# Optimization experiments

Measured on AMD Instinct MI355X. Metric: run time of the kernel, lower is better.

The kernel has to match this reference:

```python
import jax, jax.numpy as jnp
import numpy as np

GRAN = 4      # mask_spatial_granularity
STRIDE = 1    # dilate_stride
PAD = 1       # ExpandMask padding -> 3x3 all-ones dilation kernel


def setup_inputs() -> dict:
    key = jax.random.key(0)
    k1, k2, k3 = jax.random.split(key, 3)
    B, C, H, W = 32, 64, 112, 112
    G = 4
    mh, mw = H // STRIDE // GRAN, W // STRIDE // GRAN
    x = jax.random.normal(k1, (B, C, H, W), jnp.float32)
    weight = jax.random.normal(k2, (2 * G, C), jnp.float32) * 0.05  # 1x1 conv
    bias = jnp.zeros((2 * G,), jnp.float32).at[:G].set(5.0).at[G + 1:].set(1.0)
    # standard gumbel(0,1) noise for gumbel_softmax
    u = jax.random.uniform(k3, (B, 2, G, mh, mw), jnp.float32, 1e-10, 1.0)
    gumbel = -jnp.log(-jnp.log(u))
    temperature = jnp.float32(1.0)
    return {"x": x, "weight": weight, "bias": bias, "gumbel": gumbel,
            "temperature": temperature}


def reference(x, weight, bias, gumbel, temperature):
    B, C, H, W = x.shape
    G = weight.shape[0] // 2
    mh, mw = H // STRIDE // GRAN, W // STRIDE // GRAN   # mask grid (28,28)
    fh, fw = H // STRIDE, W // STRIDE                   # feature size (112,112)

    # adaptive_avg_pool2d (H,W evenly divisible by mask grid)
    m = x.reshape(B, C, mh, H // mh, mw, W // mw).mean(axis=(3, 5))
    flops = C * mh * mw
    # 1x1 conv
    m = jnp.einsum('bchw,oc->bohw', m, weight) + bias[None, :, None, None]
    flops += (weight.shape[0] * weight.shape[1] + weight.shape[1]) * mh * mw

    # gumbel_softmax over dim=1 with hard=True (straight-through)
    logits = m.reshape(B, 2, G, mh, mw)
    y_soft = jax.nn.softmax((logits + gumbel) / temperature, axis=1)
    idx = jnp.argmax(y_soft, axis=1)
    y_hard = jax.nn.one_hot(idx, 2, axis=1, dtype=y_soft.dtype)
    y = y_hard - jax.lax.stop_gradient(y_soft) + y_soft
    mask = y[:, 0]                                      # [B,G,mh,mw]
    sparsity = mask.sum() / mask.size

    # F.interpolate(size=feature_size), default mode='nearest' with integer factor
    mask = jnp.repeat(jnp.repeat(mask, fh // mh, axis=2), fw // mw, axis=3)

    # ExpandMask (stride=1): 3x3 all-ones full (cross-channel) conv, then >0.5
    dk = jnp.ones((G, G, 1 + 2 * PAD, 1 + 2 * PAD), mask.dtype)
    dil = jax.lax.conv_general_dilated(
        mask, dk, window_strides=(1, 1), padding=((PAD, PAD), (PAD, PAD)),
        dimension_numbers=('NCHW', 'OIHW', 'NCHW'))
    mask_dil = dil > 0.5
    sparsity_dil = jnp.mean(mask_dil.astype(jnp.float32))

    return mask, mask_dil, sparsity, sparsity_dil, flops
```

## Files before the change

kernel.cpp:

```cpp
#include <hip/hip_runtime.h>

#define MH 28
#define MW 28
#define CC 64
#define GG 4
#define NB 32


__global__ __launch_bounds__(256) void masker_stage1(
    const float* __restrict__ x, const float* __restrict__ w,
    const float* __restrict__ bias, const float* __restrict__ gum,
    unsigned char* __restrict__ coarse, unsigned char* __restrict__ anyb)
{
    int b  = blockIdx.x / MH;
    int ch = blockIdx.x % MH;
    int t  = threadIdx.x;

    __shared__ float pooled[CC][MW];
    __shared__ float wlds[8 * CC];
    __shared__ float logits[8][MW];
    __shared__ unsigned char mlds[GG][MW];

    float g0 = 0.f, g1 = 0.f, bo = 0.f;
    if (t < GG * MW) {
        int g = t / MW, cw = t - g * MW;
        g0 = gum[((((size_t)b * 2 + 0) * GG + g) * MH + ch) * MW + cw];
        g1 = gum[((((size_t)b * 2 + 1) * GG + g) * MH + ch) * MW + cw];
    }
    if (t < 8 * MW) bo = bias[t / MW];
    if (t < 128) ((float4*)wlds)[t] = ((const float4*)w)[t];

    const float* xb = x + (size_t)b * CC * 112 * 112 + (size_t)(4 * ch) * 112;
    #pragma unroll
    for (int k = 0; k < 7; ++k) {
        int p  = t + 256 * k;
        int c  = p / MW;
        int cw = p - c * MW;
        const float* base = xb + (size_t)c * (112 * 112) + 4 * cw;
        float s = 0.f;
        #pragma unroll
        for (int hh = 0; hh < 4; ++hh) {
            float4 v = *(const float4*)(base + hh * 112);
            s += v.x + v.y + v.z + v.w;
        }
        pooled[c][cw] = s * 0.0625f;
    }
    __syncthreads();

    if (t < 8 * MW) {
        int o  = t / MW;
        int cw = t - o * MW;
        float acc = bo;
        #pragma unroll
        for (int c = 0; c < CC; ++c)
            acc += pooled[c][cw] * wlds[o * CC + c];
        logits[o][cw] = acc;
    }
    __syncthreads();

    if (t < GG * MW) {
        int g  = t / MW;
        int cw = t - g * MW;
        unsigned char mv = (logits[g][cw] + g0 >= logits[g + 4][cw] + g1) ? 1u : 0u;
        mlds[g][cw] = mv;
        coarse[(((size_t)b * GG + g) * MH + ch) * MW + cw] = mv;
    }
    __syncthreads();
    if (t < MW) {
        unsigned char a = mlds[0][t] | mlds[1][t] | mlds[2][t] | mlds[3][t];
        anyb[((size_t)b * MH + ch) * MW + t] = a;
    }
}

__global__ __launch_bounds__(256) void masker_stage2(
    const unsigned char* __restrict__ coarse,
    const unsigned char* __restrict__ anyb,
    float* __restrict__ out_mask, float* __restrict__ out_dil,
    uint2* __restrict__ slots)
{
    int b  = blockIdx.x / MH;
    int ch = blockIdx.x % MH;
    int t  = threadIdx.x;

    __shared__ float carr[GG][MW];
    __shared__ float R[3][MW + 2];
    __shared__ unsigned int sm[4], sd[4];

    unsigned int local_m = 0;
    if (t < GG * MW) {
        int g = t / MW; int cw = t - g * MW;
        unsigned char mv = coarse[(((size_t)b * GG + g) * MH + ch) * MW + cw];
        carr[g][cw] = (float)mv;
        local_m = mv;
    }
    if (t < MW) {
        float a  = (float)anyb[((size_t)b * MH + ch) * MW + t];
        float am = (ch > 0)      ? (float)anyb[((size_t)b * MH + ch - 1) * MW + t] : 0.f;
        float ap = (ch < MH - 1) ? (float)anyb[((size_t)b * MH + ch + 1) * MW + t] : 0.f;
        R[0][t + 1] = fmaxf(a, am);
        R[1][t + 1] = a;
        R[2][t + 1] = fmaxf(a, ap);
    }
    if (t < 3) { R[t][0] = 0.f; R[t][MW + 1] = 0.f; }
    __syncthreads();

    unsigned int local_d = 0;
    #pragma unroll
    for (int k = 0; k < 7; ++k) {
        int idx = t + 256 * k;
        int g   = idx / 448;
        int rem = idx - g * 448;
        int hh  = rem / 112;
        int wfi = rem - hh * 112;
        int cw  = wfi >> 2;
        int wm  = wfi & 3;
        int rv  = (hh == 0) ? 0 : (hh == 3 ? 2 : 1);
        float d;
        if (wm == 0)      d = fmaxf(R[rv][cw],     R[rv][cw + 1]);
        else if (wm == 3) d = fmaxf(R[rv][cw + 1], R[rv][cw + 2]);
        else              d = R[rv][cw + 1];
        float mv = carr[g][cw];
        size_t o = (((size_t)b * GG + g) * 112 + (4 * ch + hh)) * 112 + wfi;
        out_mask[o] = mv;
        out_dil[o]  = d;
        local_d += (d > 0.5f) ? 1u : 0u;
    }

    #pragma unroll
    for (int off = 32; off; off >>= 1) {
        local_m += __shfl_down(local_m, off);
        local_d += __shfl_down(local_d, off);
    }
    if ((t & 63) == 0) { sm[t >> 6] = local_m; sd[t >> 6] = local_d; }
    __syncthreads();
    if (t == 0) {
        uint2 v;
        v.x = sm[0] + sm[1] + sm[2] + sm[3];
        v.y = sd[0] + sd[1] + sd[2] + sd[3];
        slots[blockIdx.x] = v;
    }
}

__global__ __launch_bounds__(256) void masker_stage3(
    const uint2* __restrict__ slots, float* __restrict__ out_scalars)
{
    int t = threadIdx.x;
    unsigned int m = 0, d = 0;
    for (int i = t; i < NB * MH; i += 256) {
        uint2 v = slots[i];
        m += v.x; d += v.y;
    }
    #pragma unroll
    for (int off = 32; off; off >>= 1) {
        m += __shfl_down(m, off);
        d += __shfl_down(d, off);
    }
    __shared__ unsigned int sm[4], sd[4];
    if ((t & 63) == 0) { sm[t >> 6] = m; sd[t >> 6] = d; }
    __syncthreads();
    if (t == 0) {
        unsigned int tm = sm[0] + sm[1] + sm[2] + sm[3];
        unsigned int td = sd[0] + sd[1] + sd[2] + sd[3];
        out_scalars[0] = (float)tm / 100352.0f;
        out_scalars[1] = (float)td / 1605632.0f;
        out_scalars[2] = 501760.0f;
    }
}

extern "C" void kernel_launch(void* const* d_in, const int* in_sizes, int n_in,
                              void* d_out, int out_size, void* d_ws, size_t ws_size,
                              hipStream_t stream) {
    const float* x    = (const float*)d_in[0];
    const float* w    = (const float*)d_in[1];
    const float* bias = (const float*)d_in[2];
    const float* gum  = (const float*)d_in[3];

    float* out = (float*)d_out;
    const size_t n_mask = (size_t)NB * GG * 112 * 112;

    uint2*         slots  = (uint2*)d_ws;
    unsigned char* coarse = (unsigned char*)d_ws + 8192;
    unsigned char* anyb   = (unsigned char*)d_ws + 8192 + 100352;

    dim3 grid(NB * MH);
    masker_stage1<<<grid, 256, 0, stream>>>(x, w, bias, gum, coarse, anyb);
    masker_stage2<<<grid, 256, 0, stream>>>(coarse, anyb,
                                            out, out + n_mask, slots);
    masker_stage3<<<1, 256, 0, stream>>>(slots, out + 2 * n_mask);
}
```

Baseline: 30.56 us.

## Split pooling across channel groups and fuse decision, dilation and reduction kernels

The pooling/1x1-conv stage is split into four channel-group blocks per mask row, writing partial logits, which quadruples the grid and the parallelism for the bandwidth-bound read of x. A second kernel sums the partials, applies gumbel and decision for the row and its neighbours (recomputing halo rows rather than reading a stored any-mask), writes outputs, and finishes the global sparsity with atomic counters and a last-block pattern. This removes the third launch in exchange for redundant halo computation, an extra partial-logit buffer, and atomics, with the counters reset inside the first kernel.

Result: slower. 58.87 us (+92.6%).

```diff
diff --git a/kernel.cpp b/kernel.cpp
--- a/kernel.cpp
+++ b/kernel.cpp
@@ -5,101 +5,117 @@
 #define CC 64
 #define GG 4
 #define NB 32
+#define CSPLIT 4
+#define CHP 16
 
 
-__global__ __launch_bounds__(256) void masker_stage1(
+__global__ __launch_bounds__(256) void masker_pool(
     const float* __restrict__ x, const float* __restrict__ w,
-    const float* __restrict__ bias, const float* __restrict__ gum,
-    unsigned char* __restrict__ coarse, unsigned char* __restrict__ anyb)
+    float* __restrict__ plog, unsigned int* __restrict__ cnts)
 {
-    int b  = blockIdx.x / MH;
-    int ch = blockIdx.x % MH;
-    int t  = threadIdx.x;
+    int blk = blockIdx.x;
+    int sp  = blk & 3;
+    int bc  = blk >> 2;
+    int b   = bc / MH;
+    int ch  = bc - b * MH;
+    int t   = threadIdx.x;
 
-    __shared__ float pooled[CC][MW];
-    __shared__ float wlds[8 * CC];
-    __shared__ float logits[8][MW];
-    __shared__ unsigned char mlds[GG][MW];
+    if (blk == 0 && t < 3) cnts[t] = 0u;
 
-    float g0 = 0.f, g1 = 0.f, bo = 0.f;
-    if (t < GG * MW) {
-        int g = t / MW, cw = t - g * MW;
-        g0 = gum[((((size_t)b * 2 + 0) * GG + g) * MH + ch) * MW + cw];
-        g1 = gum[((((size_t)b * 2 + 1) * GG + g) * MH + ch) * MW + cw];
+    __shared__ float pooled[CHP][MW];
+    __shared__ float wlds[8][CHP];
+
+    if (t < 32) {
+        int o = t >> 2, q = t & 3;
+        float4 v = *(const float4*)(w + o * CC + sp * CHP + q * 4);
+        wlds[o][q * 4 + 0] = v.x; wlds[o][q * 4 + 1] = v.y;
+        wlds[o][q * 4 + 2] = v.z; wlds[o][q * 4 + 3] = v.w;
     }
-    if (t < 8 * MW) bo = bias[t / MW];
-    if (t < 128) ((float4*)wlds)[t] = ((const float4*)w)[t];
 
-    const float* xb = x + (size_t)b * CC * 112 * 112 + (size_t)(4 * ch) * 112;
+    const float* xb = x + ((size_t)b * CC + sp * CHP) * (112 * 112)
+                        + (size_t)(4 * ch) * 112;
     #pragma unroll
-    for (int k = 0; k < 7; ++k) {
-        int p  = t + 256 * k;
-        int c  = p / MW;
-        int cw = p - c * MW;
-        const float* base = xb + (size_t)c * (112 * 112) + 4 * cw;
-        float s = 0.f;
-        #pragma unroll
-        for (int hh = 0; hh < 4; ++hh) {
-            float4 v = *(const float4*)(base + hh * 112);
-            s += v.x + v.y + v.z + v.w;
+    for (int k = 0; k < 2; ++k) {
+        int p = t + 256 * k;
+        if (p < 448) {
+            int c  = p / MW;
+            int cw = p - c * MW;
+            const float* base = xb + (size_t)c * (112 * 112) + 4 * cw;
+            float s = 0.f;
+            #pragma unroll
+            for (int hh = 0; hh < 4; ++hh) {
+                float4 v = *(const float4*)(base + hh * 112);
+                s += v.x + v.y + v.z + v.w;
+            }
+            pooled[c][cw] = s * 0.0625f;
         }
-        pooled[c][cw] = s * 0.0625f;
     }
     __syncthreads();
 
     if (t < 8 * MW) {
         int o  = t / MW;
         int cw = t - o * MW;
-        float acc = bo;
+        float acc = 0.f;
         #pragma unroll
-        for (int c = 0; c < CC; ++c)
-            acc += pooled[c][cw] * wlds[o * CC + c];
-        logits[o][cw] = acc;
+        for (int c = 0; c < CHP; ++c)
+            acc += pooled[c][cw] * wlds[o][c];
+        plog[((size_t)bc * CSPLIT + sp) * 224 + t] = acc;
+    }
+}
+
+__global__ __launch_bounds__(256) void masker_fuse(
+    const float* __restrict__ plog, const float* __restrict__ bias,
+    const float* __restrict__ gum,
+    float* __restrict__ out_mask, float* __restrict__ out_dil,
+    unsigned int* __restrict__ cnts, float* __restrict__ out_scalars)
+{
+    int blk = blockIdx.x;
+    int b   = blk / MH;
+    int ch  = blk - b * MH;
+    int t   = threadIdx.x;
+
+    __shared__ float L[3][8][MW];
+    __shared__ float dec[3][GG][MW];
+    __shared__ float R[3][MW + 2];
+    __shared__ unsigned int sm[4], sd[4];
+
+    for (int idx = t; idx < 3 * 224; idx += 256) {
+        int r = idx / 224, j = idx - r * 224;
+        int row = ch - 1 + r;
+        float acc = bias[j / MW];
+        if (row >= 0 && row < MH) {
+            const float* p = plog + (size_t)(b * MH + row) * CSPLIT * 224 + j;
+            acc += p[0] + p[224] + p[448] + p[672];
+        }
+        L[r][j / MW][j % MW] = acc;
     }
     __syncthreads();
 
-    if (t < GG * MW) {
-        int g  = t / MW;
-        int cw = t - g * MW;
-        unsigned char mv = (logits[g][cw] + g0 >= logits[g + 4][cw] + g1) ? 1u : 0u;
-        mlds[g][cw] = mv;
-        coarse[(((size_t)b * GG + g) * MH + ch) * MW + cw] = mv;
+    for (int idx = t; idx < 3 * GG * MW; idx += 256) {
+        int r = idx / (GG * MW), rem = idx - r * (GG * MW);
+        int g = rem / MW, cw = rem - g * MW;
+        int row = ch - 1 + r;
+        float d = 0.f;
+        if (row >= 0 && row < MH) {
+            float g0 = gum[((((size_t)b * 2 + 0) * GG + g) * MH + row) * MW + cw];
+            float g1 = gum[((((size_t)b * 2 + 1) * GG + g) * MH + row) * MW + cw];
+            d = (L[r][g][cw] + g0 >= L[r][g + 4][cw] + g1) ? 1.f : 0.f;
+        }
+        dec[r][g][cw] = d;
     }
     __syncthreads();
-    if (t < MW) {
-        unsigned char a = mlds[0][t] | mlds[1][t] | mlds[2][t] | mlds[3][t];
-        anyb[((size_t)b * MH + ch) * MW + t] = a;
-    }
-}
-
-__global__ __launch_bounds__(256) void masker_stage2(
-    const unsigned char* __restrict__ coarse,
-    const unsigned char* __restrict__ anyb,
-    float* __restrict__ out_mask, float* __restrict__ out_dil,
-    uint2* __restrict__ slots)
-{
-    int b  = blockIdx.x / MH;
-    int ch = blockIdx.x % MH;
-    int t  = threadIdx.x;
-
-    __shared__ float carr[GG][MW];
-    __shared__ float R[3][MW + 2];
-    __shared__ unsigned int sm[4], sd[4];
 
     unsigned int local_m = 0;
-    if (t < GG * MW) {
-        int g = t / MW; int cw = t - g * MW;
-        unsigned char mv = coarse[(((size_t)b * GG + g) * MH + ch) * MW + cw];
-        carr[g][cw] = (float)mv;
-        local_m = mv;
-    }
+    if (t < GG * MW)
+        local_m = (unsigned int)dec[1][t / MW][t - (t / MW) * MW];
+
     if (t < MW) {
-        float a  = (float)anyb[((size_t)b * MH + ch) * MW + t];
-        float am = (ch > 0)      ? (float)anyb[((size_t)b * MH + ch - 1) * MW + t] : 0.f;
-        float ap = (ch < MH - 1) ? (float)anyb[((size_t)b * MH + ch + 1) * MW + t] : 0.f;
-        R[0][t + 1] = fmaxf(a, am);
-        R[1][t + 1] = a;
-        R[2][t + 1] = fmaxf(a, ap);
+        float a0 = fmaxf(fmaxf(dec[0][0][t], dec[0][1][t]), fmaxf(dec[0][2][t], dec[0][3][t]));
+        float a1 = fmaxf(fmaxf(dec[1][0][t], dec[1][1][t]), fmaxf(dec[1][2][t], dec[1][3][t]));
+        float a2 = fmaxf(fmaxf(dec[2][0][t], dec[2][1][t]), fmaxf(dec[2][2][t], dec[2][3][t]));
+        R[0][t + 1] = fmaxf(a1, a0);
+        R[1][t + 1] = a1;
+        R[2][t + 1] = fmaxf(a1, a2);
     }
     if (t < 3) { R[t][0] = 0.f; R[t][MW + 1] = 0.f; }
     __syncthreads();
@@ -119,7 +135,7 @@
         if (wm == 0)      d = fmaxf(R[rv][cw],     R[rv][cw + 1]);
         else if (wm == 3) d = fmaxf(R[rv][cw + 1], R[rv][cw + 2]);
         else              d = R[rv][cw + 1];
-        float mv = carr[g][cw];
+        float mv = dec[1][g][cw];
         size_t o = (((size_t)b * GG + g) * 112 + (4 * ch + hh)) * 112 + wfi;
         out_mask[o] = mv;
         out_dil[o]  = d;
@@ -133,37 +149,21 @@
     }
     if ((t & 63) == 0) { sm[t >> 6] = local_m; sd[t >> 6] = local_d; }
     __syncthreads();
+
     if (t == 0) {
-        uint2 v;
-        v.x = sm[0] + sm[1] + sm[2] + sm[3];
-        v.y = sd[0] + sd[1] + sd[2] + sd[3];
-        slots[blockIdx.x] = v;
-    }
-}
-
-__global__ __launch_bounds__(256) void masker_stage3(
-    const uint2* __restrict__ slots, float* __restrict__ out_scalars)
-{
-    int t = threadIdx.x;
-    unsigned int m = 0, d = 0;
-    for (int i = t; i < NB * MH; i += 256) {
-        uint2 v = slots[i];
-        m += v.x; d += v.y;
-    }
-    #pragma unroll
-    for (int off = 32; off; off >>= 1) {
-        m += __shfl_down(m, off);
-        d += __shfl_down(d, off);
-    }
-    __shared__ unsigned int sm[4], sd[4];
-    if ((t & 63) == 0) { sm[t >> 6] = m; sd[t >> 6] = d; }
-    __syncthreads();
-    if (t == 0) {
-        unsigned int tm = sm[0] + sm[1] + sm[2] + sm[3];
-        unsigned int td = sd[0] + sd[1] + sd[2] + sd[3];
-        out_scalars[0] = (float)tm / 100352.0f;
-        out_scalars[1] = (float)td / 1605632.0f;
-        out_scalars[2] = 501760.0f;
+        unsigned int bm = sm[0] + sm[1] + sm[2] + sm[3];
+        unsigned int bd = sd[0] + sd[1] + sd[2] + sd[3];
+        atomicAdd(&cnts[0], bm);
+        atomicAdd(&cnts[1], bd);
+        __threadfence();
+        unsigned int prev = atomicAdd(&cnts[2], 1u);
+        if (prev == NB * MH - 1) {
+            unsigned int tm = atomicAdd(&cnts[0], 0u);
+            unsigned int td = atomicAdd(&cnts[1], 0u);
+            out_scalars[0] = (float)tm / 100352.0f;
+            out_scalars[1] = (float)td / 1605632.0f;
+            out_scalars[2] = 501760.0f;
+        }
     }
 }
 
@@ -178,13 +178,11 @@
     float* out = (float*)d_out;
     const size_t n_mask = (size_t)NB * GG * 112 * 112;
 
-    uint2*         slots  = (uint2*)d_ws;
-    unsigned char* coarse = (unsigned char*)d_ws + 8192;
-    unsigned char* anyb   = (unsigned char*)d_ws + 8192 + 100352;
+    unsigned int* cnts = (unsigned int*)d_ws;
+    float*        plog = (float*)((char*)d_ws + 256);
 
-    dim3 grid(NB * MH);
-    masker_stage1<<<grid, 256, 0, stream>>>(x, w, bias, gum, coarse, anyb);
-    masker_stage2<<<grid, 256, 0, stream>>>(coarse, anyb,
-                                            out, out + n_mask, slots);
-    masker_stage3<<<1, 256, 0, stream>>>(slots, out + 2 * n_mask);
+    masker_pool<<<dim3(NB * MH * CSPLIT), 256, 0, stream>>>(x, w, plog, cnts);
+    masker_fuse<<<dim3(NB * MH), 256, 0, stream>>>(plog, bias, gum,
+                                                   out, out + n_mask,
+                                                   cnts, out + 2 * n_mask);
 }
```

## Fold scalar reduction into stage-2 via dedicated reducer block, drop third kernel

Applied to the files above, without the earlier changes.

Removes the third single-block reduction kernel and the per-block slot writes. Block 0 of the second kernel now computes both sparsity totals straight from the coarse mask bytes and the any-group map. It counts dilated pixels analytically from the 3x3 neighbourhood rather than summing the expanded output. This saves one kernel launch and the cross-block slot traffic, at the cost of a serial per-row scan in one block that may become the tail of the grid.

After: 46.37 us. +51.7%, slower.

```diff
diff --git a/kernel.cpp b/kernel.cpp
--- a/kernel.cpp
+++ b/kernel.cpp
@@ -6,16 +6,15 @@
 #define GG 4
 #define NB 32
 
+#define COARSE_OFF 0
+#define ANYB_OFF   100864
 
-__global__ __launch_bounds__(256) void masker_stage1(
+__global__ __launch_bounds__(256) void masker_d1(
     const float* __restrict__ x, const float* __restrict__ w,
     const float* __restrict__ bias, const float* __restrict__ gum,
     unsigned char* __restrict__ coarse, unsigned char* __restrict__ anyb)
 {
-    int b  = blockIdx.x / MH;
-    int ch = blockIdx.x % MH;
-    int t  = threadIdx.x;
-
+    int b = blockIdx.x / MH, ch = blockIdx.x % MH, t = threadIdx.x;
     __shared__ float pooled[CC][MW];
     __shared__ float wlds[8 * CC];
     __shared__ float logits[8][MW];
@@ -33,9 +32,7 @@
     const float* xb = x + (size_t)b * CC * 112 * 112 + (size_t)(4 * ch) * 112;
     #pragma unroll
     for (int k = 0; k < 7; ++k) {
-        int p  = t + 256 * k;
-        int c  = p / MW;
-        int cw = p - c * MW;
+        int p = t + 256 * k, c = p / MW, cw = p - c * MW;
         const float* base = xb + (size_t)c * (112 * 112) + 4 * cw;
         float s = 0.f;
         #pragma unroll
@@ -46,52 +43,104 @@
         pooled[c][cw] = s * 0.0625f;
     }
     __syncthreads();
-
     if (t < 8 * MW) {
-        int o  = t / MW;
-        int cw = t - o * MW;
+        int o = t / MW, cw = t - o * MW;
         float acc = bo;
         #pragma unroll
-        for (int c = 0; c < CC; ++c)
-            acc += pooled[c][cw] * wlds[o * CC + c];
+        for (int c = 0; c < CC; ++c) acc += pooled[c][cw] * wlds[o * CC + c];
         logits[o][cw] = acc;
     }
     __syncthreads();
-
     if (t < GG * MW) {
-        int g  = t / MW;
-        int cw = t - g * MW;
+        int g = t / MW, cw = t - g * MW;
         unsigned char mv = (logits[g][cw] + g0 >= logits[g + 4][cw] + g1) ? 1u : 0u;
         mlds[g][cw] = mv;
         coarse[(((size_t)b * GG + g) * MH + ch) * MW + cw] = mv;
     }
     __syncthreads();
-    if (t < MW) {
-        unsigned char a = mlds[0][t] | mlds[1][t] | mlds[2][t] | mlds[3][t];
-        anyb[((size_t)b * MH + ch) * MW + t] = a;
-    }
+    if (t < MW)
+        anyb[((size_t)b * MH + ch) * MW + t] =
+            mlds[0][t] | mlds[1][t] | mlds[2][t] | mlds[3][t];
 }
 
-__global__ __launch_bounds__(256) void masker_stage2(
+__global__ __launch_bounds__(256) void masker_d2(
     const unsigned char* __restrict__ coarse,
     const unsigned char* __restrict__ anyb,
     float* __restrict__ out_mask, float* __restrict__ out_dil,
-    uint2* __restrict__ slots)
+    float* __restrict__ out_scalars)
 {
-    int b  = blockIdx.x / MH;
-    int ch = blockIdx.x % MH;
-    int t  = threadIdx.x;
+    const int t = threadIdx.x;
+
+    if (blockIdx.x == 0) {
+        __shared__ unsigned int sm[4], sd[4];
+
+        unsigned int accw = 0;
+        const uint4* cw4 = (const uint4*)coarse;
+        for (int i = t; i < 6272; i += 256) {
+            uint4 v = cw4[i];
+            accw += v.x + v.y + v.z + v.w;
+        }
+        unsigned int local_m = (accw & 0xFF) + ((accw >> 8) & 0xFF)
+                             + ((accw >> 16) & 0xFF) + ((accw >> 24) & 0xFF);
+
+        unsigned int local_d = 0;
+        #pragma unroll
+        for (int it = 0; it < 4; ++it) {
+            int pair = t + 256 * it;
+            if (pair < NB * MH) {
+                int b  = pair / MH, ch = pair - (pair / MH) * MH;
+                const unsigned char* r1 = anyb + (size_t)b * MH * MW + ch * MW;
+                const unsigned char* r0 = (ch > 0)      ? r1 - MW : 0;
+                const unsigned char* r2 = (ch < MH - 1) ? r1 + MW : 0;
+                int e0p = 0, mip = 0, e1p = 0;
+                int a   = r1[0];
+                int e0c = a | (r0 ? r0[0] : 0);
+                int mic = a;
+                int e1c = a | (r2 ? r2[0] : 0);
+                unsigned int cnt = 0;
+                for (int cw = 0; cw < MW; ++cw) {
+                    int e0n = 0, min_ = 0, e1n = 0;
+                    if (cw + 1 < MW) {
+                        int an = r1[cw + 1];
+                        e0n = an | (r0 ? r0[cw + 1] : 0);
+                        min_ = an;
+                        e1n = an | (r2 ? r2[cw + 1] : 0);
+                    }
+                    cnt += (unsigned)((e0p | e0c) + 2 * e0c + (e0c | e0n));
+                    cnt += (unsigned)(2 * ((mip | mic) + 2 * mic + (mic | min_)));
+                    cnt += (unsigned)((e1p | e1c) + 2 * e1c + (e1c | e1n));
+                    e0p = e0c; mip = mic; e1p = e1c;
+                    e0c = e0n; mic = min_; e1c = e1n;
+                }
+                local_d += cnt;
+            }
+        }
+
+        #pragma unroll
+        for (int off = 32; off; off >>= 1) {
+            local_m += __shfl_down(local_m, off);
+            local_d += __shfl_down(local_d, off);
+        }
+        if ((t & 63) == 0) { sm[t >> 6] = local_m; sd[t >> 6] = local_d; }
+        __syncthreads();
+        if (t == 0) {
+            out_scalars[0] = (float)(sm[0] + sm[1] + sm[2] + sm[3]) / 100352.0f;
+            out_scalars[1] = (float)(sd[0] + sd[1] + sd[2] + sd[3]) / 1605632.0f;
+            out_scalars[2] = 501760.0f;
+        }
+        return;
+    }
+
+    const int blk = blockIdx.x - 1;
+    const int b   = blk / MH;
+    const int ch  = blk - b * MH;
 
     __shared__ float carr[GG][MW];
     __shared__ float R[3][MW + 2];
-    __shared__ unsigned int sm[4], sd[4];
 
-    unsigned int local_m = 0;
     if (t < GG * MW) {
-        int g = t / MW; int cw = t - g * MW;
-        unsigned char mv = coarse[(((size_t)b * GG + g) * MH + ch) * MW + cw];
-        carr[g][cw] = (float)mv;
-        local_m = mv;
+        int g = t / MW, cw = t - g * MW;
+        carr[g][cw] = (float)coarse[(((size_t)b * GG + g) * MH + ch) * MW + cw];
     }
     if (t < MW) {
         float a  = (float)anyb[((size_t)b * MH + ch) * MW + t];
@@ -104,7 +153,6 @@
     if (t < 3) { R[t][0] = 0.f; R[t][MW + 1] = 0.f; }
     __syncthreads();
 
-    unsigned int local_d = 0;
     #pragma unroll
     for (int k = 0; k < 7; ++k) {
         int idx = t + 256 * k;
@@ -123,47 +171,6 @@
         size_t o = (((size_t)b * GG + g) * 112 + (4 * ch + hh)) * 112 + wfi;
         out_mask[o] = mv;
         out_dil[o]  = d;
-        local_d += (d > 0.5f) ? 1u : 0u;
-    }
-
-    #pragma unroll
-    for (int off = 32; off; off >>= 1) {
-        local_m += __shfl_down(local_m, off);
-        local_d += __shfl_down(local_d, off);
-    }
-    if ((t & 63) == 0) { sm[t >> 6] = local_m; sd[t >> 6] = local_d; }
-    __syncthreads();
-    if (t == 0) {
-        uint2 v;
-        v.x = sm[0] + sm[1] + sm[2] + sm[3];
-        v.y = sd[0] + sd[1] + sd[2] + sd[3];
-        slots[blockIdx.x] = v;
-    }
-}
-
-__global__ __launch_bounds__(256) void masker_stage3(
-    const uint2* __restrict__ slots, float* __restrict__ out_scalars)
-{
-    int t = threadIdx.x;
-    unsigned int m = 0, d = 0;
-    for (int i = t; i < NB * MH; i += 256) {
-        uint2 v = slots[i];
-        m += v.x; d += v.y;
-    }
-    #pragma unroll
-    for (int off = 32; off; off >>= 1) {
-        m += __shfl_down(m, off);
-        d += __shfl_down(d, off);
-    }
-    __shared__ unsigned int sm[4], sd[4];
-    if ((t & 63) == 0) { sm[t >> 6] = m; sd[t >> 6] = d; }
-    __syncthreads();
-    if (t == 0) {
-        unsigned int tm = sm[0] + sm[1] + sm[2] + sm[3];
-        unsigned int td = sd[0] + sd[1] + sd[2] + sd[3];
-        out_scalars[0] = (float)tm / 100352.0f;
-        out_scalars[1] = (float)td / 1605632.0f;
-        out_scalars[2] = 501760.0f;
     }
 }
 
@@ -178,13 +185,11 @@
     float* out = (float*)d_out;
     const size_t n_mask = (size_t)NB * GG * 112 * 112;
 
-    uint2*         slots  = (uint2*)d_ws;
-    unsigned char* coarse = (unsigned char*)d_ws + 8192;
-    unsigned char* anyb   = (unsigned char*)d_ws + 8192 + 100352;
+    unsigned char* coarse = (unsigned char*)d_ws + COARSE_OFF;
+    unsigned char* anyb   = (unsigned char*)d_ws + ANYB_OFF;
 
-    dim3 grid(NB * MH);
-    masker_stage1<<<grid, 256, 0, stream>>>(x, w, bias, gum, coarse, anyb);
-    masker_stage2<<<grid, 256, 0, stream>>>(coarse, anyb,
-                                            out, out + n_mask, slots);
-    masker_stage3<<<1, 256, 0, stream>>>(slots, out + 2 * n_mask);
+    masker_d1<<<dim3(NB * MH), 256, 0, stream>>>(x, w, bias, gum, coarse, anyb);
+    masker_d2<<<dim3(NB * MH + 1), 256, 0, stream>>>(coarse, anyb,
+                                                     out, out + n_mask,
+                                                     out + 2 * n_mask);
 }
```
